# Optimization experiments

Measured on AMD Instinct MI355X. Metric: run time of the kernel, lower is better.

The kernel has to match this reference:

```python
import jax, jax.numpy as jnp
import numpy as np

N_HEADS = 32
N_KV_HEADS = 8
HEAD_DIM = 128
N_REP = N_HEADS // N_KV_HEADS


def _apply_rope(t, cos, sin):
    # t: [b, s, h, d]; cos/sin: [s, d//2]
    tr = t[..., 0::2]
    ti = t[..., 1::2]
    c = cos[None, :, None, :]
    s = sin[None, :, None, :]
    out_r = tr * c - ti * s
    out_i = tr * s + ti * c
    # interleave back: (..., d//2, 2) -> (..., d)
    return jnp.stack([out_r, out_i], axis=-1).reshape(t.shape)


def setup_inputs() -> dict:
    key = jax.random.key(0)
    ks = jax.random.split(key, 8)
    bsz, seqlen, dim = 2, 2048, 4096
    kv_dim = N_KV_HEADS * HEAD_DIM
    x = jax.random.normal(ks[0], (bsz, seqlen, dim), dtype=jnp.float32)
    # rotary frequencies as in llama: theta=10000
    half = HEAD_DIM // 2
    inv_freq = 1.0 / (10000.0 ** (np.arange(0, half, dtype=np.float32) / half))
    pos = np.arange(seqlen, dtype=np.float32)
    ang = np.outer(pos, inv_freq)  # [s, d//2]
    freqs_cos = jnp.asarray(np.cos(ang), dtype=jnp.float32)
    freqs_sin = jnp.asarray(np.sin(ang), dtype=jnp.float32)
    # causal additive mask [s, s]
    neg_inf = jnp.finfo(jnp.float32).min
    mask = jnp.where(jnp.tril(jnp.ones((seqlen, seqlen), dtype=bool)), 0.0, neg_inf).astype(jnp.float32)
    sc = 1.0 / np.sqrt(dim)
    wq = jax.random.normal(ks[1], (dim, dim), dtype=jnp.float32) * sc
    wk = jax.random.normal(ks[2], (kv_dim, dim), dtype=jnp.float32) * sc
    wv = jax.random.normal(ks[3], (kv_dim, dim), dtype=jnp.float32) * sc
    wo = jax.random.normal(ks[4], (dim, dim), dtype=jnp.float32) * sc
    return {"x": x, "mask": mask, "freqs_cos": freqs_cos, "freqs_sin": freqs_sin,
            "wq": wq, "wk": wk, "wv": wv, "wo": wo, "start_pos": 0}


def reference(x, mask, freqs_cos, freqs_sin, wq, wk, wv, wo, start_pos):
    bsz, seqlen, dim = x.shape
    xq = jnp.einsum('bsd,od->bso', x, wq).reshape(bsz, seqlen, N_HEADS, HEAD_DIM)
    xk = jnp.einsum('bsd,od->bso', x, wk).reshape(bsz, seqlen, N_KV_HEADS, HEAD_DIM)
    xv = jnp.einsum('bsd,od->bso', x, wv).reshape(bsz, seqlen, N_KV_HEADS, HEAD_DIM)
    xq = _apply_rope(xq, freqs_cos[:seqlen], freqs_sin[:seqlen])
    xk = _apply_rope(xk, freqs_cos[:seqlen], freqs_sin[:seqlen])
    # KV cache: positions [0, start_pos) are zeros (fresh cache), then the new keys/values
    if start_pos > 0:
        zpad = jnp.zeros((bsz, start_pos, N_KV_HEADS, HEAD_DIM), dtype=xk.dtype)
        keys = jnp.concatenate([zpad, xk], axis=1)
        values = jnp.concatenate([zpad, xv], axis=1)
    else:
        keys, values = xk, xv
    # GQA expansion
    keys = jnp.repeat(keys, N_REP, axis=2)     # [b, kv_len, H, d]
    values = jnp.repeat(values, N_REP, axis=2)
    q = xq.transpose(0, 2, 1, 3)               # [b, H, s, d]
    k = keys.transpose(0, 2, 1, 3)
    v = values.transpose(0, 2, 1, 3)
    scores = jnp.einsum('bhqd,bhkd->bhqk', q, k) / np.sqrt(HEAD_DIM)
    kv_len = scores.shape[-1]
    m = mask
    if m.shape[-1] != kv_len:  # pad with -inf on the right like F.pad(value=-inf)
        neg_inf = jnp.finfo(scores.dtype).min
        m = jnp.pad(m, ((0, 0), (0, kv_len - m.shape[-1])), constant_values=neg_inf)
    scores = scores + m[None, None, :, :]
    probs = jax.nn.softmax(scores, axis=-1)
    out = jnp.einsum('bhqk,bhkd->bhqd', probs, v)
    out = out.transpose(0, 2, 1, 3).reshape(bsz, seqlen, N_HEADS * HEAD_DIM)
    return jnp.einsum('bso,do->bsd', out, wo)
```

## Files before the change

### kernel.cpp

```cpp
#include <hip/hip_runtime.h>
#include <cstdint>
#include <cstddef>

typedef unsigned short u16;
typedef short s8v __attribute__((ext_vector_type(8)));
typedef float f4v __attribute__((ext_vector_type(4)));

#define DEV static __device__ __forceinline__

DEV float bf2f(u16 u) {
  union { unsigned int i; float f; } v; v.i = ((unsigned int)u) << 16; return v.f;
}
DEV u16 f2bf(float f) {
  union { unsigned int i; float f; } v; v.f = f;
  unsigned int r = v.i + 0x7fffu + ((v.i >> 16) & 1u);
  return (u16)(r >> 16);
}

DEV void load_lds16(const u16* g, u16* l) {
  __builtin_amdgcn_global_load_lds((const __attribute__((address_space(1))) void*)g,
                                   (__attribute__((address_space(3))) void*)l, 16, 0, 0);
}

DEV f4v mfma16(s8v a, s8v b, f4v c) {
  return __builtin_amdgcn_mfma_f32_16x16x32_bf16(a, b, c, 0, 0, 0);
}

__global__ __launch_bounds__(256)
void cvt_all(const float* __restrict__ x,  const float* __restrict__ wq,
             const float* __restrict__ wk, const float* __restrict__ wv,
             const float* __restrict__ wo, u16* __restrict__ dst)
{
  const size_t NB = (size_t)4096 * 4096;
  const size_t KV = (size_t)4096 * 1024;
  const size_t gi = ((size_t)blockIdx.x * 256 + threadIdx.x) * 4;
  const float* src;
  size_t li;
  if (gi < NB)                { src = x;  li = gi; }
  else if (gi < 2 * NB)       { src = wq; li = gi - NB; }
  else if (gi < 2 * NB + KV)  { src = wk; li = gi - 2 * NB; }
  else if (gi < 2 * NB + 2*KV){ src = wv; li = gi - 2 * NB - KV; }
  else                        { src = wo; li = gi - 2 * NB - 2 * KV; }
  const float4 v = *(const float4*)(src + li);
  u16 o[4] = { f2bf(v.x), f2bf(v.y), f2bf(v.z), f2bf(v.w) };
  *(ushort4*)(dst + gi) = *(ushort4*)o;
}

DEV void storec(float* p, float v) { *p = v; }
DEV void storec(u16* p, float v)   { *p = f2bf(v); }

#define BARR  __builtin_amdgcn_s_barrier()
#define LGKM0 asm volatile("s_waitcnt lgkmcnt(0)" ::: "memory")
#define WVM4  asm volatile("s_waitcnt vmcnt(4)" ::: "memory")
#define WVM2  asm volatile("s_waitcnt vmcnt(2)" ::: "memory")
#define WVM0  asm volatile("s_waitcnt vmcnt(0)" ::: "memory")
#define MEMF  asm volatile("" ::: "memory")
#define PRIO1 __builtin_amdgcn_s_setprio(1)
#define PRIO0 __builtin_amdgcn_s_setprio(0)

template <typename TC>
__global__ __launch_bounds__(512, 2)
void gemm_256(const u16* __restrict__ A, const u16* __restrict__ Bt,
              TC* __restrict__ C, int M, int N, int K)
{
  __shared__ u16 lA[2][2][8192];
  __shared__ u16 lB[2][2][8192];

  const int tid  = threadIdx.x;
  const int wid  = tid >> 6;
  const int lane = tid & 63;
  const int quad = lane >> 4;
  const int l16  = lane & 15;
  const int wr   = wid >> 2;
  const int wc   = wid & 3;
  const int r0   = blockIdx.y * 256;
  const int c0   = blockIdx.x * 256;

  const int srow = tid >> 3;
  const int scol = (((tid & 7) ^ ((tid >> 3) & 7)) << 3);
  const u16* pA = A  + (size_t)(r0 + srow) * K + scol;
  const u16* pB = Bt + (size_t)(c0 + srow) * K + scol;
  const size_t h64  = (size_t)64 * K;
  const size_t h128 = (size_t)128 * K;

  const int swz = (l16 & 7) << 3;
  const int ko0 = (quad * 8) ^ swz;
  const int ko1 = (32 + quad * 8) ^ swz;

  f4v acc[2][2][4][2];
#pragma unroll
  for (int a = 0; a < 2; ++a)
#pragma unroll
    for (int b = 0; b < 2; ++b)
#pragma unroll
      for (int c = 0; c < 4; ++c)
#pragma unroll
        for (int d = 0; d < 2; ++d) acc[a][b][c][d] = (f4v)0.0f;

  s8v af[4][2], b0f[2][2], b1f[2][2];

#define STG_A(BUF, H, K0) do {                                  \
    const u16* g = pA + (size_t)(H) * h128 + (K0);              \
    load_lds16(g,       &lA[BUF][H][wid * 512]);                \
    load_lds16(g + h64, &lA[BUF][H][wid * 512 + 4096]);         \
  } while (0)
#define STG_B(BUF, H, K0) do {                                  \
    const u16* g = pB + (size_t)(H) * h128 + (K0);              \
    load_lds16(g,       &lB[BUF][H][wid * 512]);                \
    load_lds16(g + h64, &lB[BUF][H][wid * 512 + 4096]);         \
  } while (0)

#define RD_A(BUF, MH) do {                                      \
    _Pragma("unroll")                                           \
    for (int mi = 0; mi < 4; ++mi) {                            \
      const int lr = wr * 64 + mi * 16 + l16;                   \
      af[mi][0] = *(const s8v*)&lA[BUF][MH][lr * 64 + ko0];     \
      af[mi][1] = *(const s8v*)&lA[BUF][MH][lr * 64 + ko1];     \
    } } while (0)
#define RD_B(BUF, NH, DST) do {                                 \
    _Pragma("unroll")                                           \
    for (int ni = 0; ni < 2; ++ni) {                            \
      const int lr = wc * 32 + ni * 16 + l16;                   \
      DST[ni][0] = *(const s8v*)&lB[BUF][NH][lr * 64 + ko0];    \
      DST[ni][1] = *(const s8v*)&lB[BUF][NH][lr * 64 + ko1];    \
    } } while (0)

#define MF(MH, NH, BF) do {                                     \
    _Pragma("unroll")                                           \
    for (int mi = 0; mi < 4; ++mi)                              \
      _Pragma("unroll")                                         \
      for (int ni = 0; ni < 2; ++ni) {                          \
        acc[MH][NH][mi][ni] = mfma16(af[mi][0], BF[ni][0], acc[MH][NH][mi][ni]); \
        acc[MH][NH][mi][ni] = mfma16(af[mi][1], BF[ni][1], acc[MH][NH][mi][ni]); \
      } } while (0)

#define TILE(BUF, KN)                                                     \
  RD_A(BUF, 0); RD_B(BUF, 0, b0f); STG_A(BUF ^ 1, 0, KN);                 \
  BARR; LGKM0; PRIO1; MF(0, 0, b0f); PRIO0; WVM4; BARR;                   \
  RD_B(BUF, 1, b1f); STG_B(BUF ^ 1, 0, KN);                               \
  BARR; LGKM0; PRIO1; MF(0, 1, b1f); PRIO0; WVM4; BARR;                   \
  RD_A(BUF, 1); STG_B(BUF ^ 1, 1, KN);                                    \
  BARR; LGKM0; PRIO1; MF(1, 0, b0f); PRIO0; MEMF; BARR;                   \
  STG_A(BUF ^ 1, 1, KN);                                                  \
  BARR; LGKM0; PRIO1; MF(1, 1, b1f); PRIO0; WVM4; BARR;

#define FTILE(BUF)                                                        \
  RD_A(BUF, 0); RD_B(BUF, 0, b0f);                                        \
  BARR; LGKM0; PRIO1; MF(0, 0, b0f); PRIO0; WVM2; BARR;                   \
  RD_B(BUF, 1, b1f);                                                      \
  BARR; LGKM0; PRIO1; MF(0, 1, b1f); PRIO0; WVM0; BARR;                   \
  RD_A(BUF, 1);                                                           \
  BARR; LGKM0; PRIO1; MF(1, 0, b0f); PRIO0; MEMF; BARR;                   \
  PRIO1; MF(1, 1, b1f); PRIO0;

  STG_A(0, 0, 0); STG_B(0, 0, 0); STG_B(0, 1, 0); STG_A(0, 1, 0);
  WVM4; BARR;

  const int NT = K >> 6;
  for (int kt = 0; kt < NT - 2; kt += 2) {
    const int ka = (kt + 1) << 6;
    const int kb = (kt + 2) << 6;
    TILE(0, ka);
    TILE(1, kb);
  }
  TILE(0, (NT - 1) << 6);
  FTILE(1);

#pragma unroll
  for (int mh = 0; mh < 2; ++mh)
#pragma unroll
    for (int nh = 0; nh < 2; ++nh)
#pragma unroll
      for (int mi = 0; mi < 4; ++mi)
#pragma unroll
        for (int ni = 0; ni < 2; ++ni) {
          const int col = c0 + nh * 128 + wc * 32 + ni * 16 + l16;
#pragma unroll
          for (int reg = 0; reg < 4; ++reg) {
            const int row = r0 + mh * 128 + wr * 64 + mi * 16 + quad * 4 + reg;
            storec(&C[(size_t)row * N + col], acc[mh][nh][mi][ni][reg]);
          }
        }
#undef STG_A
#undef STG_B
#undef RD_A
#undef RD_B
#undef MF
#undef TILE
#undef FTILE
}

DEV void stage8(const float* g, u16* dst) {
  const float4 a = *(const float4*)g;
  const float4 b = *(const float4*)(g + 4);
  u16 t[8] = { f2bf(a.x), f2bf(a.y), f2bf(a.z), f2bf(a.w),
               f2bf(b.x), f2bf(b.y), f2bf(b.z), f2bf(b.w) };
  *(s8v*)dst = *(s8v*)t;
}
DEV void stage8(const u16* g, u16* dst) {
  *(s8v*)dst = *(const s8v*)g;
}

template <typename TA, typename TB, typename TC>
__global__ __launch_bounds__(256)
void gemm_bt_f(const TA* __restrict__ A, const TB* __restrict__ Bt,
               TC* __restrict__ C, int M, int N, int K)
{
  __shared__ u16 lds_a[128 * 32];
  __shared__ u16 lds_b[128 * 32];

  const int tid  = threadIdx.x;
  const int w    = tid >> 6;
  const int lane = tid & 63;
  const int quad = lane >> 4;
  const int l16  = lane & 15;
  const int bm   = blockIdx.y;
  const int bn   = blockIdx.x;
  const int wm   = (w >> 1) * 64;
  const int wn   = (w & 1) * 64;

  const int srow = tid >> 2;
  const int scol = (tid & 3) * 8;

  const TA* ga0 = A  + ((size_t)(bm * 128 + srow)) * K + scol;
  const TB* gb0 = Bt + ((size_t)(bn * 128 + srow)) * K + scol;
  const TA* ga1 = ga0 + (size_t)64 * K;
  const TB* gb1 = gb0 + (size_t)64 * K;

  f4v acc[4][4];
#pragma unroll
  for (int i = 0; i < 4; ++i)
#pragma unroll
    for (int j = 0; j < 4; ++j) acc[i][j] = (f4v)0.0f;

  for (int k0 = 0; k0 < K; k0 += 32) {
    stage8(ga0 + k0, &lds_a[tid * 8]);
    stage8(ga1 + k0, &lds_a[2048 + tid * 8]);
    stage8(gb0 + k0, &lds_b[tid * 8]);
    stage8(gb1 + k0, &lds_b[2048 + tid * 8]);
    __syncthreads();

    s8v af[4], bf[4];
#pragma unroll
    for (int mi = 0; mi < 4; ++mi)
      af[mi] = *(const s8v*)&lds_a[(wm + mi * 16 + l16) * 32 + quad * 8];
#pragma unroll
    for (int ni = 0; ni < 4; ++ni)
      bf[ni] = *(const s8v*)&lds_b[(wn + ni * 16 + l16) * 32 + quad * 8];
#pragma unroll
    for (int mi = 0; mi < 4; ++mi)
#pragma unroll
      for (int ni = 0; ni < 4; ++ni)
        acc[mi][ni] = __builtin_amdgcn_mfma_f32_16x16x32_bf16(af[mi], bf[ni], acc[mi][ni], 0, 0, 0);
    __syncthreads();
  }

#pragma unroll
  for (int mi = 0; mi < 4; ++mi)
#pragma unroll
    for (int ni = 0; ni < 4; ++ni) {
      const int col = bn * 128 + wn + ni * 16 + l16;
#pragma unroll
      for (int reg = 0; reg < 4; ++reg) {
        const int row = bm * 128 + wm + mi * 16 + quad * 4 + reg;
        storec(&C[(size_t)row * N + col], acc[mi][ni][reg]);
      }
    }
}

__global__ __launch_bounds__(256)
void rope_kernel(u16* __restrict__ t, const float* __restrict__ cs,
                 const float* __restrict__ sn, int heads, int rowstride)
{
  const int idx = blockIdx.x * 256 + threadIdx.x;
  const int ppr = heads * 64;
  const int row = idx / ppr;
  const int rem = idx - row * ppr;
  const int head = rem >> 6;
  const int pr   = rem & 63;
  const int pos  = row & 2047;
  const float c = cs[pos * 64 + pr];
  const float s = sn[pos * 64 + pr];
  unsigned int* p = (unsigned int*)(t + (size_t)row * rowstride + head * 128 + pr * 2);
  const unsigned int v = *p;
  const float xr = bf2f((u16)(v & 0xffffu));
  const float xi = bf2f((u16)(v >> 16));
  const u16 o0 = f2bf(xr * c - xi * s);
  const u16 o1 = f2bf(xr * s + xi * c);
  *p = (unsigned int)o0 | ((unsigned int)o1 << 16);
}

__global__ __launch_bounds__(512)
void flash_attn128(const u16* __restrict__ xq, const u16* __restrict__ xk,
                   const u16* __restrict__ xv, u16* __restrict__ out, int kvstride)
{
  const int bx  = (int)gridDim.x - 1 - (int)blockIdx.x;
  const int h   = blockIdx.y;
  const int b   = blockIdx.z;
  const int kvh = h >> 2;

  const int tid  = threadIdx.x;
  const int w    = tid >> 6;
  const int lane = tid & 63;
  const int quad = lane >> 4;
  const int l16  = lane & 15;

  __shared__ u16 kt[2][64 * 128];
  __shared__ u16 vt[128 * 72];
  __shared__ u16 pb[8][16 * 72];

  const u16* qp = xq + ((size_t)(b * 2048 + bx * 128 + w * 16 + l16)) * 4096 + h * 128 + quad * 8;
  s8v qf[4];
#pragma unroll
  for (int ks = 0; ks < 4; ++ks) qf[ks] = *(const s8v*)(qp + ks * 32);

  f4v oa[8];
#pragma unroll
  for (int i = 0; i < 8; ++i) oa[i] = (f4v)0.0f;
  float l_part[4] = {0.0f, 0.0f, 0.0f, 0.0f};

  const int krow = w * 4 + (lane >> 4);
  const int ksw  = ((lane & 15) ^ (krow & 7)) * 8;
  const int vkv2 = (tid & 31) * 2;
  const int vdg  = tid >> 5;

  const u16* kbase = xk + (size_t)(b * 2048) * kvstride + kvh * 128;
  const u16* vbase = xv + (size_t)(b * 2048) * kvstride + kvh * 128;

  const float scale = 0.08838834764831845f;
  const float MFIX  = 8.0f;

  const int nkb   = 2 * bx + 2;
  const int qmaxw = bx * 128 + w * 16 + 15;
  const int swz   = l16 & 7;

  s8v vr[2];
  {
    const u16* vg = vbase + (size_t)vkv2 * kvstride + vdg * 8;
    vr[0] = *(const s8v*)(vg);
    vr[1] = *(const s8v*)(vg + kvstride);
    const u16* kg = kbase + (size_t)krow * kvstride + ksw;
    load_lds16(kg, &kt[0][w * 512]);
    load_lds16(kg + (size_t)32 * kvstride, &kt[0][w * 512 + 4096]);
  }

  for (int kb = 0; kb < nkb; ++kb) {
    BARR;
    WVM2;
#pragma unroll
    for (int j = 0; j < 8; ++j) {
      const int d = vdg * 8 + j;
      *(unsigned int*)&vt[d * 72 + vkv2] =
          (unsigned int)(u16)vr[0][j] | ((unsigned int)(u16)vr[1][j] << 16);
    }
    if (kb + 1 < nkb) {
      const u16* vg = vbase + (size_t)((kb + 1) * 64 + vkv2) * kvstride + vdg * 8;
      vr[0] = *(const s8v*)(vg);
      vr[1] = *(const s8v*)(vg + kvstride);
      const u16* kg = kbase + (size_t)((kb + 1) * 64 + krow) * kvstride + ksw;
      u16* dst = &kt[(kb + 1) & 1][w * 512];
      load_lds16(kg, dst);
      load_lds16(kg + (size_t)32 * kvstride, dst + 4096);
      WVM4;
    } else {
      WVM0;
    }
    LGKM0;
    BARR;
    const u16* ktc = &kt[kb & 1][0];

    if (kb * 64 <= qmaxw) {
      f4v sa[4];
#pragma unroll
      for (int nb = 0; nb < 4; ++nb) sa[nb] = (f4v)0.0f;
      __builtin_amdgcn_s_setprio(1);
#pragma unroll
      for (int nb = 0; nb < 4; ++nb)
#pragma unroll
        for (int ks = 0; ks < 4; ++ks) {
          const s8v kf = *(const s8v*)&ktc[(nb * 16 + l16) * 128 + ((ks * 4 + quad) ^ swz) * 8];
          sa[nb] = __builtin_amdgcn_mfma_f32_16x16x32_bf16(qf[ks], kf, sa[nb], 0, 0, 0);
        }
      __builtin_amdgcn_s_setprio(0);

#pragma unroll
      for (int nb = 0; nb < 4; ++nb)
#pragma unroll
        for (int reg = 0; reg < 4; ++reg) {
          const int kvg  = kb * 64 + nb * 16 + l16;
          const int qpos = bx * 128 + w * 16 + quad * 4 + reg;
          float p = 0.0f;
          if (kvg <= qpos) p = __expf(fmaf(sa[nb][reg], scale, -MFIX));
          l_part[reg] += p;
          pb[w][(quad * 4 + reg) * 72 + nb * 16 + l16] = f2bf(p);
        }

      s8v pf[2];
#pragma unroll
      for (int ks = 0; ks < 2; ++ks)
        pf[ks] = *(const s8v*)&pb[w][l16 * 72 + ks * 32 + quad * 8];
      __builtin_amdgcn_s_setprio(1);
#pragma unroll
      for (int d8 = 0; d8 < 8; ++d8)
#pragma unroll
        for (int ks = 0; ks < 2; ++ks) {
          const s8v vf = *(const s8v*)&vt[(d8 * 16 + l16) * 72 + ks * 32 + quad * 8];
          oa[d8] = __builtin_amdgcn_mfma_f32_16x16x32_bf16(pf[ks], vf, oa[d8], 0, 0, 0);
        }
      __builtin_amdgcn_s_setprio(0);
    }
  }

#pragma unroll
  for (int reg = 0; reg < 4; ++reg) {
    float l = l_part[reg];
    l += __shfl_xor(l, 1);
    l += __shfl_xor(l, 2);
    l += __shfl_xor(l, 4);
    l += __shfl_xor(l, 8);
    const float inv = 1.0f / l;
    const int row = bx * 128 + w * 16 + quad * 4 + reg;
    u16* op = out + ((size_t)(b * 2048 + row)) * 4096 + h * 128 + l16;
#pragma unroll
    for (int d8 = 0; d8 < 8; ++d8)
      op[d8 * 16] = f2bf(oa[d8][reg] * inv);
  }
}

extern "C" void kernel_launch(void* const* d_in, const int* in_sizes, int n_in,
                              void* d_out, int out_size, void* d_ws, size_t ws_size,
                              hipStream_t stream)
{
  const float* x  = (const float*)d_in[0];
  const float* fc = (const float*)d_in[2];
  const float* fs = (const float*)d_in[3];
  const float* wq = (const float*)d_in[4];
  const float* wk = (const float*)d_in[5];
  const float* wv = (const float*)d_in[6];
  const float* wo = (const float*)d_in[7];

  const size_t NE_BIG = (size_t)4096 * 4096;
  const size_t NE_KV  = (size_t)4096 * 1024;

  u16* xq = (u16*)d_out;
  u16* xk = (u16*)d_ws;
  u16* xv = xk + NE_KV;
  u16* ao = xv + NE_KV;
  u16* xb  = ao + NE_BIG;
  u16* wqb = xb  + NE_BIG;
  u16* wkb = wqb + NE_BIG;
  u16* wvb = wkb + NE_KV;
  u16* wob = wvb + NE_KV;

  const size_t need_fast = (size_t)((wob + NE_BIG) - (u16*)d_ws) * sizeof(u16);

  if (ws_size >= need_fast) {
    cvt_all<<<57344, 256, 0, stream>>>(x, wq, wk, wv, wo, xb);
    gemm_256<u16><<<dim3(16, 16), 512, 0, stream>>>(xb, wqb, xq, 4096, 4096, 4096);
    gemm_256<u16><<<dim3(8, 16),  512, 0, stream>>>(xb, wkb, xk, 4096, 2048, 4096);
    rope_kernel<<<32768, 256, 0, stream>>>(xq, fc, fs, 32, 4096);
    rope_kernel<<<8192,  256, 0, stream>>>(xk, fc, fs, 8, 2048);
    flash_attn128<<<dim3(16, 32, 2), 512, 0, stream>>>(xq, xk, xk + 1024, ao, 2048);
    gemm_256<float><<<dim3(16, 16), 512, 0, stream>>>(ao, wob, (float*)d_out, 4096, 4096, 4096);
  } else {
    gemm_bt_f<float, float, u16><<<dim3(32, 32), 256, 0, stream>>>(x, wq, xq, 4096, 4096, 4096);
    gemm_bt_f<float, float, u16><<<dim3(8, 32),  256, 0, stream>>>(x, wk, xk, 4096, 1024, 4096);
    gemm_bt_f<float, float, u16><<<dim3(8, 32),  256, 0, stream>>>(x, wv, xv, 4096, 1024, 4096);
    rope_kernel<<<32768, 256, 0, stream>>>(xq, fc, fs, 32, 4096);
    rope_kernel<<<8192,  256, 0, stream>>>(xk, fc, fs, 8, 1024);
    flash_attn128<<<dim3(16, 32, 2), 512, 0, stream>>>(xq, xk, xv, ao, 1024);
    gemm_bt_f<u16, float, float><<<dim3(32, 32), 256, 0, stream>>>(ao, wo, (float*)d_out, 4096, 4096, 4096);
  }
}
```

Baseline: 784.0 us.

## Halve flash-attention block to 4 waves, each handling two 16-row query tiles

The attention kernel now runs 256 threads per block instead of 512. Each wave processes two 16-row query sub-tiles (rows offset by 64), so every K fragment read from LDS and every V fragment feeds two MFMAs. K/V tile loads per thread double to keep the same 64-row KV block, and the vmcnt waits are adjusted to match. The aim is to cut LDS traffic per MFMA and allow two blocks per CU, at the cost of more registers per thread. The causal skip check now uses the upper half's max row, so lower-half waves do extra masked work on diagonal blocks.

```diff
diff --git a/kernel.cpp b/kernel.cpp
--- a/kernel.cpp
+++ b/kernel.cpp
@@ -51,6 +51,7 @@
 
 #define BARR  __builtin_amdgcn_s_barrier()
 #define LGKM0 asm volatile("s_waitcnt lgkmcnt(0)" ::: "memory")
+#define WVM8  asm volatile("s_waitcnt vmcnt(8)" ::: "memory")
 #define WVM4  asm volatile("s_waitcnt vmcnt(4)" ::: "memory")
 #define WVM2  asm volatile("s_waitcnt vmcnt(2)" ::: "memory")
 #define WVM0  asm volatile("s_waitcnt vmcnt(0)" ::: "memory")
@@ -290,7 +291,7 @@
   *p = (unsigned int)o0 | ((unsigned int)o1 << 16);
 }
 
-__global__ __launch_bounds__(512)
+__global__ __launch_bounds__(256, 2)
 void flash_attn128(const u16* __restrict__ xq, const u16* __restrict__ xk,
                    const u16* __restrict__ xv, u16* __restrict__ out, int kvstride)
 {
@@ -307,20 +308,24 @@
 
   __shared__ u16 kt[2][64 * 128];
   __shared__ u16 vt[128 * 72];
-  __shared__ u16 pb[8][16 * 72];
-
-  const u16* qp = xq + ((size_t)(b * 2048 + bx * 128 + w * 16 + l16)) * 4096 + h * 128 + quad * 8;
-  s8v qf[4];
-#pragma unroll
-  for (int ks = 0; ks < 4; ++ks) qf[ks] = *(const s8v*)(qp + ks * 32);
-
-  f4v oa[8];
-#pragma unroll
-  for (int i = 0; i < 8; ++i) oa[i] = (f4v)0.0f;
-  float l_part[4] = {0.0f, 0.0f, 0.0f, 0.0f};
-
-  const int krow = w * 4 + (lane >> 4);
-  const int ksw  = ((lane & 15) ^ (krow & 7)) * 8;
+  __shared__ u16 pb[4][16 * 72];
+
+  s8v qf[2][4];
+#pragma unroll
+  for (int hf = 0; hf < 2; ++hf) {
+    const u16* qp = xq + ((size_t)(b * 2048 + bx * 128 + hf * 64 + w * 16 + l16)) * 4096
+                  + h * 128 + quad * 8;
+#pragma unroll
+    for (int ks = 0; ks < 4; ++ks) qf[hf][ks] = *(const s8v*)(qp + ks * 32);
+  }
+
+  f4v oa[2][8];
+#pragma unroll
+  for (int hf = 0; hf < 2; ++hf)
+#pragma unroll
+    for (int i = 0; i < 8; ++i) oa[hf][i] = (f4v)0.0f;
+  float l_part[2][4] = {{0.f,0.f,0.f,0.f},{0.f,0.f,0.f,0.f}};
+
   const int vkv2 = (tid & 31) * 2;
   const int vdg  = tid >> 5;
 
@@ -331,37 +336,50 @@
   const float MFIX  = 8.0f;
 
   const int nkb   = 2 * bx + 2;
-  const int qmaxw = bx * 128 + w * 16 + 15;
+  const int qmax1 = bx * 128 + 64 + w * 16 + 15;
   const int swz   = l16 & 7;
 
-  s8v vr[2];
+  s8v vr[4];
   {
-    const u16* vg = vbase + (size_t)vkv2 * kvstride + vdg * 8;
+    const u16* vg = vbase + (size_t)vkv2 * kvstride + vdg * 16;
     vr[0] = *(const s8v*)(vg);
-    vr[1] = *(const s8v*)(vg + kvstride);
-    const u16* kg = kbase + (size_t)krow * kvstride + ksw;
-    load_lds16(kg, &kt[0][w * 512]);
-    load_lds16(kg + (size_t)32 * kvstride, &kt[0][w * 512 + 4096]);
+    vr[1] = *(const s8v*)(vg + 8);
+    vr[2] = *(const s8v*)(vg + kvstride);
+    vr[3] = *(const s8v*)(vg + kvstride + 8);
+#pragma unroll
+    for (int i = 0; i < 4; ++i) {
+      const int row = w * 16 + i * 4 + (lane >> 4);
+      const u16* kg = kbase + (size_t)row * kvstride + (((lane & 15) ^ (row & 7)) << 3);
+      load_lds16(kg, &kt[0][w * 2048 + i * 512]);
+    }
   }
 
   for (int kb = 0; kb < nkb; ++kb) {
     BARR;
-    WVM2;
-#pragma unroll
-    for (int j = 0; j < 8; ++j) {
-      const int d = vdg * 8 + j;
-      *(unsigned int*)&vt[d * 72 + vkv2] =
-          (unsigned int)(u16)vr[0][j] | ((unsigned int)(u16)vr[1][j] << 16);
-    }
+    WVM4;
+#pragma unroll
+    for (int di = 0; di < 2; ++di)
+#pragma unroll
+      for (int j = 0; j < 8; ++j) {
+        const int d = vdg * 16 + di * 8 + j;
+        *(unsigned int*)&vt[d * 72 + vkv2] =
+            (unsigned int)(u16)vr[di][j] | ((unsigned int)(u16)vr[2 + di][j] << 16);
+      }
     if (kb + 1 < nkb) {
-      const u16* vg = vbase + (size_t)((kb + 1) * 64 + vkv2) * kvstride + vdg * 8;
+      const u16* vg = vbase + (size_t)((kb + 1) * 64 + vkv2) * kvstride + vdg * 16;
       vr[0] = *(const s8v*)(vg);
-      vr[1] = *(const s8v*)(vg + kvstride);
-      const u16* kg = kbase + (size_t)((kb + 1) * 64 + krow) * kvstride + ksw;
-      u16* dst = &kt[(kb + 1) & 1][w * 512];
-      load_lds16(kg, dst);
-      load_lds16(kg + (size_t)32 * kvstride, dst + 4096);
-      WVM4;
+      vr[1] = *(const s8v*)(vg + 8);
+      vr[2] = *(const s8v*)(vg + kvstride);
+      vr[3] = *(const s8v*)(vg + kvstride + 8);
+      u16* dstb = &kt[(kb + 1) & 1][0];
+#pragma unroll
+      for (int i = 0; i < 4; ++i) {
+        const int row = w * 16 + i * 4 + (lane >> 4);
+        const u16* kg = kbase + (size_t)((kb + 1) * 64 + row) * kvstride
+                      + (((lane & 15) ^ (row & 7)) << 3);
+        load_lds16(kg, dstb + w * 2048 + i * 512);
+      }
+      WVM8;
     } else {
       WVM0;
     }
@@ -369,20 +387,22 @@
     BARR;
     const u16* ktc = &kt[kb & 1][0];
 
-    if (kb * 64 <= qmaxw) {
-      f4v sa[4];
-#pragma unroll
-      for (int nb = 0; nb < 4; ++nb) sa[nb] = (f4v)0.0f;
+    if (kb * 64 <= qmax1) {
+      f4v sa0[4], sa1[4];
+#pragma unroll
+      for (int nb = 0; nb < 4; ++nb) { sa0[nb] = (f4v)0.0f; sa1[nb] = (f4v)0.0f; }
       __builtin_amdgcn_s_setprio(1);
 #pragma unroll
       for (int nb = 0; nb < 4; ++nb)
 #pragma unroll
         for (int ks = 0; ks < 4; ++ks) {
           const s8v kf = *(const s8v*)&ktc[(nb * 16 + l16) * 128 + ((ks * 4 + quad) ^ swz) * 8];
-          sa[nb] = __builtin_amdgcn_mfma_f32_16x16x32_bf16(qf[ks], kf, sa[nb], 0, 0, 0);
+          sa0[nb] = __builtin_amdgcn_mfma_f32_16x16x32_bf16(qf[0][ks], kf, sa0[nb], 0, 0, 0);
+          sa1[nb] = __builtin_amdgcn_mfma_f32_16x16x32_bf16(qf[1][ks], kf, sa1[nb], 0, 0, 0);
         }
       __builtin_amdgcn_s_setprio(0);
 
+      s8v pf0[2], pf1[2];
 #pragma unroll
       for (int nb = 0; nb < 4; ++nb)
 #pragma unroll
@@ -390,41 +410,57 @@
           const int kvg  = kb * 64 + nb * 16 + l16;
           const int qpos = bx * 128 + w * 16 + quad * 4 + reg;
           float p = 0.0f;
-          if (kvg <= qpos) p = __expf(fmaf(sa[nb][reg], scale, -MFIX));
-          l_part[reg] += p;
+          if (kvg <= qpos) p = __expf(fmaf(sa0[nb][reg], scale, -MFIX));
+          l_part[0][reg] += p;
           pb[w][(quad * 4 + reg) * 72 + nb * 16 + l16] = f2bf(p);
         }
-
-      s8v pf[2];
 #pragma unroll
       for (int ks = 0; ks < 2; ++ks)
-        pf[ks] = *(const s8v*)&pb[w][l16 * 72 + ks * 32 + quad * 8];
+        pf0[ks] = *(const s8v*)&pb[w][l16 * 72 + ks * 32 + quad * 8];
+#pragma unroll
+      for (int nb = 0; nb < 4; ++nb)
+#pragma unroll
+        for (int reg = 0; reg < 4; ++reg) {
+          const int kvg  = kb * 64 + nb * 16 + l16;
+          const int qpos = bx * 128 + 64 + w * 16 + quad * 4 + reg;
+          float p = 0.0f;
+          if (kvg <= qpos) p = __expf(fmaf(sa1[nb][reg], scale, -MFIX));
+          l_part[1][reg] += p;
+          pb[w][(quad * 4 + reg) * 72 + nb * 16 + l16] = f2bf(p);
+        }
+#pragma unroll
+      for (int ks = 0; ks < 2; ++ks)
+        pf1[ks] = *(const s8v*)&pb[w][l16 * 72 + ks * 32 + quad * 8];
+
       __builtin_amdgcn_s_setprio(1);
 #pragma unroll
       for (int d8 = 0; d8 < 8; ++d8)
 #pragma unroll
         for (int ks = 0; ks < 2; ++ks) {
           const s8v vf = *(const s8v*)&vt[(d8 * 16 + l16) * 72 + ks * 32 + quad * 8];
-          oa[d8] = __builtin_amdgcn_mfma_f32_16x16x32_bf16(pf[ks], vf, oa[d8], 0, 0, 0);
+          oa[0][d8] = __builtin_amdgcn_mfma_f32_16x16x32_bf16(pf0[ks], vf, oa[0][d8], 0, 0, 0);
+          oa[1][d8] = __builtin_amdgcn_mfma_f32_16x16x32_bf16(pf1[ks], vf, oa[1][d8], 0, 0, 0);
         }
       __builtin_amdgcn_s_setprio(0);
     }
   }
 
 #pragma unroll
-  for (int reg = 0; reg < 4; ++reg) {
-    float l = l_part[reg];
-    l += __shfl_xor(l, 1);
-    l += __shfl_xor(l, 2);
-    l += __shfl_xor(l, 4);
-    l += __shfl_xor(l, 8);
-    const float inv = 1.0f / l;
-    const int row = bx * 128 + w * 16 + quad * 4 + reg;
-    u16* op = out + ((size_t)(b * 2048 + row)) * 4096 + h * 128 + l16;
-#pragma unroll
-    for (int d8 = 0; d8 < 8; ++d8)
-      op[d8 * 16] = f2bf(oa[d8][reg] * inv);
-  }
+  for (int hf = 0; hf < 2; ++hf)
+#pragma unroll
+    for (int reg = 0; reg < 4; ++reg) {
+      float l = l_part[hf][reg];
+      l += __shfl_xor(l, 1);
+      l += __shfl_xor(l, 2);
+      l += __shfl_xor(l, 4);
+      l += __shfl_xor(l, 8);
+      const float inv = 1.0f / l;
+      const int row = bx * 128 + hf * 64 + w * 16 + quad * 4 + reg;
+      u16* op = out + ((size_t)(b * 2048 + row)) * 4096 + h * 128 + l16;
+#pragma unroll
+      for (int d8 = 0; d8 < 8; ++d8)
+        op[d8 * 16] = f2bf(oa[hf][d8][reg] * inv);
+    }
 }
 
 extern "C" void kernel_launch(void* const* d_in, const int* in_sizes, int n_in,
@@ -460,7 +496,7 @@
     gemm_256<u16><<<dim3(8, 16),  512, 0, stream>>>(xb, wkb, xk, 4096, 2048, 4096);
     rope_kernel<<<32768, 256, 0, stream>>>(xq, fc, fs, 32, 4096);
     rope_kernel<<<8192,  256, 0, stream>>>(xk, fc, fs, 8, 2048);
-    flash_attn128<<<dim3(16, 32, 2), 512, 0, stream>>>(xq, xk, xk + 1024, ao, 2048);
+    flash_attn128<<<dim3(16, 32, 2), 256, 0, stream>>>(xq, xk, xk + 1024, ao, 2048);
     gemm_256<float><<<dim3(16, 16), 512, 0, stream>>>(ao, wob, (float*)d_out, 4096, 4096, 4096);
   } else {
     gemm_bt_f<float, float, u16><<<dim3(32, 32), 256, 0, stream>>>(x, wq, xq, 4096, 4096, 4096);
@@ -468,7 +504,7 @@
     gemm_bt_f<float, float, u16><<<dim3(8, 32),  256, 0, stream>>>(x, wv, xv, 4096, 1024, 4096);
     rope_kernel<<<32768, 256, 0, stream>>>(xq, fc, fs, 32, 4096);
     rope_kernel<<<8192,  256, 0, stream>>>(xk, fc, fs, 8, 1024);
-    flash_attn128<<<dim3(16, 32, 2), 512, 0, stream>>>(xq, xk, xv, ao, 1024);
+    flash_attn128<<<dim3(16, 32, 2), 256, 0, stream>>>(xq, xk, xv, ao, 1024);
     gemm_bt_f<u16, float, float><<<dim3(32, 32), 256, 0, stream>>>(ao, wo, (float*)d_out, 4096, 4096, 4096);
   }
 }
```

New measurement: 798.7 us. No clear change (+1.9%).
